# Performance work log

Measured on AMD Instinct MI355X. Metric: run time of the kernel, lower is better.

The kernel has to match this reference:

```python
import jax, jax.numpy as jnp
import numpy as np


def setup_inputs() -> dict:
    key = jax.random.key(0)
    ks = jax.random.split(key, 7)
    N, D, H1, H2, M = 16384, 2048, 512, 32, 2048
    return {
        "x": jax.random.normal(ks[0], (N, D), dtype=jnp.float32),
        "W1": jax.random.normal(ks[1], (H1, D), dtype=jnp.float32) * (1.0 / np.sqrt(D)),
        "b1": jax.random.normal(ks[2], (H1,), dtype=jnp.float32) * 0.01,
        "W2": jax.random.normal(ks[3], (H2, H1), dtype=jnp.float32) * (1.0 / np.sqrt(H1)),
        "b2": jax.random.normal(ks[4], (H2,), dtype=jnp.float32) * 0.01,
        "a_memory": jax.random.normal(ks[5], (M, H2), dtype=jnp.float32),
        "n_memory": jax.random.normal(ks[6], (M, H2), dtype=jnp.float32),
    }


def reference(x, W1, b1, W2, b2, a_memory, n_memory):
    # MLP per forward(): linear -> relu -> (dropout p=0) -> linear -> (dropout p=0)
    h = jax.nn.relu(x @ W1.T + b1)          # [N, 512]
    feat = h @ W2.T + b2                     # [N, 32] (no ReLU in forward path)
    inv_d = 1.0 / feat.shape[1]
    # caption_score(mem, f) = max_j mean(mem_j * f) = max_j (mem_j . f) / 32
    a_score = jnp.max(feat @ a_memory.T, axis=1) * inv_d  # [N]
    n_score = jnp.max(feat @ n_memory.T, axis=1) * inv_d  # [N]
    return jax.nn.sigmoid(a_score - n_score)
```

## Files before the change

### kernel.cpp

```cpp
#include <hip/hip_runtime.h>
#include <hip/hip_bf16.h>

typedef __attribute__((ext_vector_type(8))) __bf16 bf16x8;
typedef __attribute__((ext_vector_type(4))) float f32x4;

#define NROWS 16384
#define DIM   2048
#define NH1   512
#define NH2   32
#define MMEM  2048
#define BK    32
#define NT    (DIM / BK)

#define W1O ((size_t)0)
#define W2O ((size_t)2097152)
#define AMO ((size_t)2129920)
#define NMO ((size_t)2260992)
#define HO  ((size_t)2392064)

__device__ __forceinline__ f32x4 mfma16(bf16x8 a, bf16x8 b, f32x4 c) {
    return __builtin_amdgcn_mfma_f32_16x16x32_bf16(a, b, c, 0, 0, 0);
}

__device__ __forceinline__ void gload_lds16(const void* g, void* l) {
    __builtin_amdgcn_global_load_lds(
        (const __attribute__((address_space(1))) void*)g,
        (__attribute__((address_space(3))) void*)l, 16, 0, 0);
}

__device__ __forceinline__ bf16x8 cvt8(f32x4 a, f32x4 b) {
    bf16x8 o;
    o[0] = (__bf16)a[0]; o[1] = (__bf16)a[1]; o[2] = (__bf16)a[2]; o[3] = (__bf16)a[3];
    o[4] = (__bf16)b[0]; o[5] = (__bf16)b[1]; o[6] = (__bf16)b[2]; o[7] = (__bf16)b[3];
    return o;
}

struct bf4 { __bf16 a, b, c, d; };

__global__ void cvt_all_kernel(const float* __restrict__ w1f, __bf16* __restrict__ w1b,
                               const float* __restrict__ w2f, __bf16* __restrict__ w2b,
                               const float* __restrict__ amf, __bf16* __restrict__ amb,
                               const float* __restrict__ nmf, __bf16* __restrict__ nmb) {
    const int g = blockIdx.x * blockDim.x + threadIdx.x;
    const int T = gridDim.x * blockDim.x;
    for (int i = g; i < (NH1 * DIM) / 4; i += T) {
        const float4 v = *reinterpret_cast<const float4*>(w1f + i * 4);
        *reinterpret_cast<bf4*>(w1b + i * 4) = { (__bf16)v.x, (__bf16)v.y, (__bf16)v.z, (__bf16)v.w };
    }
    for (int i = g; i < (NH2 * NH1) / 4; i += T) {
        const float4 v = *reinterpret_cast<const float4*>(w2f + i * 4);
        *reinterpret_cast<bf4*>(w2b + i * 4) = { (__bf16)v.x, (__bf16)v.y, (__bf16)v.z, (__bf16)v.w };
    }
    for (int i = g; i < (MMEM * NH2) / 4; i += T) {
        const float4 v = *reinterpret_cast<const float4*>(amf + i * 4);
        *reinterpret_cast<bf4*>(amb + i * 4) = { (__bf16)v.x, (__bf16)v.y, (__bf16)v.z, (__bf16)v.w };
    }
    for (int i = g; i < (MMEM * NH2) / 4; i += T) {
        const float4 v = *reinterpret_cast<const float4*>(nmf + i * 4);
        *reinterpret_cast<bf4*>(nmb + i * 4) = { (__bf16)v.x, (__bf16)v.y, (__bf16)v.z, (__bf16)v.w };
    }
}

__global__ __launch_bounds__(256, 4) void gemm1_kernel(
    const float*  __restrict__ Xf,
    const __bf16* __restrict__ W1,
    const float*  __restrict__ b1,
    __bf16* __restrict__ Hout)
{
    __shared__ float  Af[2][64 * BK];
    __shared__ __bf16 Bs[2][128 * BK];
    const int tid  = threadIdx.x;
    const int lane = tid & 63;
    const int wave = tid >> 6;
    const int b = blockIdx.x;
    const int orig = (b & 7) * 128 + (b >> 3);
    const int bn = orig & 3;
    const int bm = orig >> 2;
    const size_t brow = (size_t)bm * 64;
    const int bcol = bn * 128;
    const int wr = wave >> 1, wc = wave & 1;

    f32x4 acc[2][4];
#pragma unroll
    for (int m = 0; m < 2; ++m)
#pragma unroll
        for (int n = 0; n < 4; ++n) acc[m][n] = (f32x4){0.f, 0.f, 0.f, 0.f};

    const int aRowT = tid >> 3;
    const int cA    = (tid & 7) ^ (aRowT & 7);
    const float* aSrcBase = Xf + (brow + aRowT) * (size_t)DIM + cA * 4;
    const int bRowT = tid >> 2;
    const int cB    = (tid & 3) ^ ((tid >> 3) & 3);
    const __bf16* bSrcBase = W1 + (size_t)(bcol + bRowT) * DIM + cB * 8;

#define STAGE(T, BI)                                                          \
    {                                                                         \
        const int k0_ = (T) * BK;                                             \
        _Pragma("unroll")                                                     \
        for (int q = 0; q < 2; ++q)                                           \
            gload_lds16(aSrcBase + (size_t)q * 32 * DIM + k0_,                \
                        (char*)Af[BI] + q * 4096 + tid * 16);                 \
        _Pragma("unroll")                                                     \
        for (int q = 0; q < 2; ++q)                                           \
            gload_lds16(bSrcBase + (size_t)q * 64 * DIM + k0_,                \
                        (char*)Bs[BI] + q * 4096 + tid * 16);                 \
    }

    const int l15 = lane & 15;
    const int kc  = lane >> 4;
    const int l7  = lane & 7;
    const int rABase = wr * 32 + l15;
    const int rBBase = wc * 64 + l15;
    const int aSlot0 = ((2 * kc)     ^ l7) << 4;
    const int aSlot1 = ((2 * kc + 1) ^ l7) << 4;
    const int bSlot  = (kc ^ ((l15 >> 1) & 3)) << 4;

#define COMPUTE(BI)                                                           \
    {                                                                         \
        const char* Ac = (const char*)Af[BI];                                 \
        const char* Bc = (const char*)Bs[BI];                                 \
        bf16x8 av[2], bv[4];                                                  \
        _Pragma("unroll")                                                     \
        for (int m = 0; m < 2; ++m) {                                         \
            const int rowB = (rABase + m * 16) * 128;                         \
            f32x4 lo = *(const f32x4*)(Ac + rowB + aSlot0);                   \
            f32x4 hi = *(const f32x4*)(Ac + rowB + aSlot1);                   \
            av[m] = cvt8(lo, hi);                                             \
        }                                                                     \
        _Pragma("unroll")                                                     \
        for (int n = 0; n < 4; ++n)                                           \
            bv[n] = *(const bf16x8*)(Bc + (rBBase + n * 16) * 64 + bSlot);    \
        _Pragma("unroll")                                                     \
        for (int m = 0; m < 2; ++m)                                           \
            _Pragma("unroll")                                                 \
            for (int n = 0; n < 4; ++n)                                       \
                acc[m][n] = mfma16(av[m], bv[n], acc[m][n]);                  \
    }

    STAGE(0, 0);
    __syncthreads();

    for (int t = 0; t < NT; ++t) {
        if (t + 1 < NT) STAGE(t + 1, (t + 1) & 1);
        COMPUTE(t & 1);
        __syncthreads();
    }
#undef STAGE
#undef COMPUTE

#pragma unroll
    for (int n = 0; n < 4; ++n) {
        const int gcol = bcol + wc * 64 + n * 16 + l15;
        const float bias = b1[gcol];
#pragma unroll
        for (int m = 0; m < 2; ++m) {
            const size_t grow0 = brow + wr * 32 + m * 16 + kc * 4;
#pragma unroll
            for (int r = 0; r < 4; ++r) {
                float v = acc[m][n][r] + bias;
                v = v > 0.f ? v : 0.f;
                Hout[(grow0 + r) * NH1 + gcol] = (__bf16)v;
            }
        }
    }
}

__global__ __launch_bounds__(512) void tail_kernel(
    const __bf16* __restrict__ Hin,
    const __bf16* __restrict__ W2b,
    const float*  __restrict__ b2,
    const __bf16* __restrict__ Am,
    const __bf16* __restrict__ Nm,
    float* __restrict__ out)
{
    __shared__ __bf16 featLds[64 * 32];
    __shared__ float aMaxLds[2][64];
    __shared__ float nMaxLds[2][64];
    const int tid  = threadIdx.x;
    const int lane = tid & 63;
    const int wave = tid >> 6;
    const int rowBase = blockIdx.x * 64;
    const int l15 = lane & 15;
    const int kc  = lane >> 4;
    const int rgrp  = (wave & 3) * 16;
    const int jHalf = wave >> 2;

    if (wave < 4) {
        f32x4 acc0 = {0.f,0.f,0.f,0.f}, acc1 = {0.f,0.f,0.f,0.f};
        const size_t hrow = (size_t)(rowBase + rgrp + l15) * NH1;
#pragma unroll
        for (int kk = 0; kk < 16; ++kk) {
            bf16x8 a  = *(const bf16x8*)(Hin + hrow + kk * 32 + kc * 8);
            bf16x8 w0 = *(const bf16x8*)(W2b + (size_t)l15 * NH1 + kk * 32 + kc * 8);
            bf16x8 w1 = *(const bf16x8*)(W2b + (size_t)(16 + l15) * NH1 + kk * 32 + kc * 8);
            acc0 = mfma16(a, w0, acc0);
            acc1 = mfma16(a, w1, acc1);
        }
        const float bias0 = b2[l15], bias1 = b2[16 + l15];
#pragma unroll
        for (int r = 0; r < 4; ++r) {
            const int lr = rgrp + kc * 4 + r;
            featLds[lr * 32 + l15]      = (__bf16)(acc0[r] + bias0);
            featLds[lr * 32 + 16 + l15] = (__bf16)(acc1[r] + bias1);
        }
    }
    __syncthreads();

    const bf16x8 af = *(const bf16x8*)&featLds[(rgrp + l15) * 32 + kc * 8];

    float rmaxA[4], rmaxN[4];
#pragma unroll
    for (int r = 0; r < 4; ++r) { rmaxA[r] = -1e30f; rmaxN[r] = -1e30f; }
    const f32x4 zero = {0.f,0.f,0.f,0.f};
    const int jBase = jHalf * (MMEM / 2);
#pragma unroll 2
    for (int jt = 0; jt < (MMEM / 2) / 16; jt += 4) {
        bf16x8 ba[4], bb[4];
#pragma unroll
        for (int u = 0; u < 4; ++u) {
            const size_t off = (size_t)(jBase + (jt + u) * 16 + l15) * NH2 + kc * 8;
            ba[u] = *(const bf16x8*)(Am + off);
            bb[u] = *(const bf16x8*)(Nm + off);
        }
#pragma unroll
        for (int u = 0; u < 4; ++u) {
            f32x4 sa = mfma16(af, ba[u], zero);
            f32x4 sn = mfma16(af, bb[u], zero);
#pragma unroll
            for (int r = 0; r < 4; ++r) {
                rmaxA[r] = fmaxf(rmaxA[r], sa[r]);
                rmaxN[r] = fmaxf(rmaxN[r], sn[r]);
            }
        }
    }
#pragma unroll
    for (int off = 1; off < 16; off <<= 1) {
#pragma unroll
        for (int r = 0; r < 4; ++r) {
            rmaxA[r] = fmaxf(rmaxA[r], __shfl_xor(rmaxA[r], off, 64));
            rmaxN[r] = fmaxf(rmaxN[r], __shfl_xor(rmaxN[r], off, 64));
        }
    }
    if (l15 == 0) {
#pragma unroll
        for (int r = 0; r < 4; ++r) {
            const int row = rgrp + kc * 4 + r;
            aMaxLds[jHalf][row] = rmaxA[r];
            nMaxLds[jHalf][row] = rmaxN[r];
        }
    }
    __syncthreads();
    if (tid < 64) {
        const float ma = fmaxf(aMaxLds[0][tid], aMaxLds[1][tid]);
        const float mn = fmaxf(nMaxLds[0][tid], nMaxLds[1][tid]);
        const float d = (ma - mn) * (1.0f / 32.0f);
        out[rowBase + tid] = 1.0f / (1.0f + __expf(-d));
    }
}

extern "C" void kernel_launch(void* const* d_in, const int* in_sizes, int n_in,
                              void* d_out, int out_size, void* d_ws, size_t ws_size,
                              hipStream_t stream) {
    (void)in_sizes; (void)n_in; (void)out_size; (void)ws_size;
    const float* x  = (const float*)d_in[0];
    const float* W1 = (const float*)d_in[1];
    const float* b1 = (const float*)d_in[2];
    const float* W2 = (const float*)d_in[3];
    const float* b2 = (const float*)d_in[4];
    const float* am = (const float*)d_in[5];
    const float* nm = (const float*)d_in[6];
    float* out = (float*)d_out;
    char* ws = (char*)d_ws;
    __bf16* w1b = (__bf16*)(ws + W1O);
    __bf16* w2b = (__bf16*)(ws + W2O);
    __bf16* amb = (__bf16*)(ws + AMO);
    __bf16* nmb = (__bf16*)(ws + NMO);
    __bf16* hb  = (__bf16*)(ws + HO);

    cvt_all_kernel<<<dim3(512), dim3(256), 0, stream>>>(W1, w1b, W2, w2b, am, amb, nm, nmb);
    gemm1_kernel<<<dim3((NROWS / 64) * (NH1 / 128)), dim3(256), 0, stream>>>(x, w1b, b1, hb);
    tail_kernel<<<dim3(NROWS / 64), dim3(512), 0, stream>>>(hb, w2b, b2, amb, nmb, out);
}
```

Before: 91.66 us.

## Convert X to bf16 in registers before LDS and double the K tile

The GEMM1 kernel no longer copies fp32 X tiles straight into LDS and converts them at MFMA time. Each thread now prefetches fp32 X into registers two stages ahead, converts to bf16 and stores the swizzled bf16 tile to LDS. BK grows from 32 to 64, which halves the number of loop iterations and barriers, and the occupancy hint drops from 4 to 3 blocks. The aim is to cut LDS footprint and bandwidth for A and to spread the barrier cost over more work. The price is extra register pressure from the prefetch and lower occupancy.

```diff
diff --git a/kernel.cpp b/kernel.cpp
--- a/kernel.cpp
+++ b/kernel.cpp
@@ -9,7 +9,7 @@
 #define NH1   512
 #define NH2   32
 #define MMEM  2048
-#define BK    32
+#define BK    64
 #define NT    (DIM / BK)
 
 #define W1O ((size_t)0)
@@ -61,14 +61,14 @@
     }
 }
 
-__global__ __launch_bounds__(256, 4) void gemm1_kernel(
+__global__ __launch_bounds__(256, 3) void gemm1_kernel(
     const float*  __restrict__ Xf,
     const __bf16* __restrict__ W1,
     const float*  __restrict__ b1,
     __bf16* __restrict__ Hout)
 {
-    __shared__ float  Af[2][64 * BK];
-    __shared__ __bf16 Bs[2][128 * BK];
+    __shared__ __bf16 Ab[2][64 * BK];
+    __shared__ __bf16 Bb[2][128 * BK];
     const int tid  = threadIdx.x;
     const int lane = tid & 63;
     const int wave = tid >> 6;
@@ -86,24 +86,23 @@
 #pragma unroll
         for (int n = 0; n < 4; ++n) acc[m][n] = (f32x4){0.f, 0.f, 0.f, 0.f};
 
-    const int aRowT = tid >> 3;
-    const int cA    = (tid & 7) ^ (aRowT & 7);
-    const float* aSrcBase = Xf + (brow + aRowT) * (size_t)DIM + cA * 4;
-    const int bRowT = tid >> 2;
-    const int cB    = (tid & 3) ^ ((tid >> 3) & 3);
-    const __bf16* bSrcBase = W1 + (size_t)(bcol + bRowT) * DIM + cB * 8;
-
-#define STAGE(T, BI)                                                          \
+    const int aRow = tid >> 2;
+    const int aQ   = tid & 3;
+    const float* aSrc = Xf + (brow + aRow) * (size_t)DIM + aQ * 16;
+    const int aW0 = aRow * 128 + (((aQ * 2)     ^ (aRow & 7)) << 4);
+    const int aW1 = aRow * 128 + (((aQ * 2 + 1) ^ (aRow & 7)) << 4);
+
+    const int bRowT  = tid >> 3;
+    const int bChunk = (tid & 7) ^ (bRowT & 7);
+    const __bf16* bSrcBase = W1 + (size_t)(bcol + bRowT) * DIM + bChunk * 8;
+
+#define STAGE_B(T, BI)                                                        \
     {                                                                         \
         const int k0_ = (T) * BK;                                             \
         _Pragma("unroll")                                                     \
-        for (int q = 0; q < 2; ++q)                                           \
-            gload_lds16(aSrcBase + (size_t)q * 32 * DIM + k0_,                \
-                        (char*)Af[BI] + q * 4096 + tid * 16);                 \
-        _Pragma("unroll")                                                     \
-        for (int q = 0; q < 2; ++q)                                           \
-            gload_lds16(bSrcBase + (size_t)q * 64 * DIM + k0_,                \
-                        (char*)Bs[BI] + q * 4096 + tid * 16);                 \
+        for (int q = 0; q < 4; ++q)                                           \
+            gload_lds16(bSrcBase + (size_t)q * 32 * DIM + k0_,                \
+                        (char*)Bb[BI] + q * 4096 + tid * 16);                 \
     }
 
     const int l15 = lane & 15;
@@ -111,41 +110,62 @@
     const int l7  = lane & 7;
     const int rABase = wr * 32 + l15;
     const int rBBase = wc * 64 + l15;
-    const int aSlot0 = ((2 * kc)     ^ l7) << 4;
-    const int aSlot1 = ((2 * kc + 1) ^ l7) << 4;
-    const int bSlot  = (kc ^ ((l15 >> 1) & 3)) << 4;
 
 #define COMPUTE(BI)                                                           \
     {                                                                         \
-        const char* Ac = (const char*)Af[BI];                                 \
-        const char* Bc = (const char*)Bs[BI];                                 \
-        bf16x8 av[2], bv[4];                                                  \
+        const char* Ac = (const char*)Ab[BI];                                 \
+        const char* Bc = (const char*)Bb[BI];                                 \
         _Pragma("unroll")                                                     \
-        for (int m = 0; m < 2; ++m) {                                         \
-            const int rowB = (rABase + m * 16) * 128;                         \
-            f32x4 lo = *(const f32x4*)(Ac + rowB + aSlot0);                   \
-            f32x4 hi = *(const f32x4*)(Ac + rowB + aSlot1);                   \
-            av[m] = cvt8(lo, hi);                                             \
-        }                                                                     \
-        _Pragma("unroll")                                                     \
-        for (int n = 0; n < 4; ++n)                                           \
-            bv[n] = *(const bf16x8*)(Bc + (rBBase + n * 16) * 64 + bSlot);    \
-        _Pragma("unroll")                                                     \
-        for (int m = 0; m < 2; ++m)                                           \
+        for (int kk = 0; kk < 2; ++kk) {                                      \
+            const int slot = ((kk * 4 + kc) ^ l7) << 4;                       \
+            bf16x8 av[2], bv[4];                                              \
+            _Pragma("unroll")                                                 \
+            for (int m = 0; m < 2; ++m)                                       \
+                av[m] = *(const bf16x8*)(Ac + (rABase + m * 16) * 128 + slot);\
             _Pragma("unroll")                                                 \
             for (int n = 0; n < 4; ++n)                                       \
-                acc[m][n] = mfma16(av[m], bv[n], acc[m][n]);                  \
-    }
-
-    STAGE(0, 0);
+                bv[n] = *(const bf16x8*)(Bc + (rBBase + n * 16) * 128 + slot);\
+            _Pragma("unroll")                                                 \
+            for (int m = 0; m < 2; ++m)                                       \
+                _Pragma("unroll")                                             \
+                for (int n = 0; n < 4; ++n)                                   \
+                    acc[m][n] = mfma16(av[m], bv[n], acc[m][n]);              \
+        }                                                                     \
+    }
+
+    f32x4 pa0, pa1, pa2, pa3;
+    {
+        STAGE_B(0, 0);
+        f32x4 t0 = *(const f32x4*)(aSrc);
+        f32x4 t1 = *(const f32x4*)(aSrc + 4);
+        f32x4 t2 = *(const f32x4*)(aSrc + 8);
+        f32x4 t3 = *(const f32x4*)(aSrc + 12);
+        *(bf16x8*)((char*)Ab[0] + aW0) = cvt8(t0, t1);
+        *(bf16x8*)((char*)Ab[0] + aW1) = cvt8(t2, t3);
+        pa0 = *(const f32x4*)(aSrc + BK);
+        pa1 = *(const f32x4*)(aSrc + BK + 4);
+        pa2 = *(const f32x4*)(aSrc + BK + 8);
+        pa3 = *(const f32x4*)(aSrc + BK + 12);
+    }
     __syncthreads();
 
     for (int t = 0; t < NT; ++t) {
-        if (t + 1 < NT) STAGE(t + 1, (t + 1) & 1);
+        if (t + 1 < NT) {
+            const int nb = (t + 1) & 1;
+            STAGE_B(t + 1, nb);
+            *(bf16x8*)((char*)Ab[nb] + aW0) = cvt8(pa0, pa1);
+            *(bf16x8*)((char*)Ab[nb] + aW1) = cvt8(pa2, pa3);
+            const int tq = (t + 2 < NT) ? (t + 2) : (NT - 1);
+            const float* qs = aSrc + (size_t)tq * BK;
+            pa0 = *(const f32x4*)(qs);
+            pa1 = *(const f32x4*)(qs + 4);
+            pa2 = *(const f32x4*)(qs + 8);
+            pa3 = *(const f32x4*)(qs + 12);
+        }
         COMPUTE(t & 1);
         __syncthreads();
     }
-#undef STAGE
+#undef STAGE_B
 #undef COMPUTE
 
 #pragma unroll
```

After: 105.1 us. +14.7%, slower.
